# Optimization experiments

Measured on AMD Instinct MI355X. Metric: run time of the kernel, lower is better.

The kernel has to match this reference:

```python
import jax, jax.numpy as jnp
import numpy as np

N_NODES = 100000
N_EDGES = 1600000
NEG_SLOPE = 0.2
EPS = 1e-16


def gat_conv(x, edge_index, W, att_src, att_dst, bias, heads, out_ch, concat):
    # x: [N, F_in]; edge_index: [2, E] with edge (src j -> dst i)
    N = x.shape[0]
    src, dst = edge_index[0], edge_index[1]
    h = (x @ W).reshape(N, heads, out_ch)              # [N, H, C]
    a_src = (h * att_src[None]).sum(-1)                # [N, H]
    a_dst = (h * att_dst[None]).sum(-1)                # [N, H]
    e = a_src[src] + a_dst[dst]                        # [E, H]
    e = jnp.where(e > 0, e, NEG_SLOPE * e)             # LeakyReLU(0.2)
    # segment softmax over destination node
    m = jax.ops.segment_max(e, dst, num_segments=N)    # [N, H]
    m = jnp.where(jnp.isfinite(m), m, 0.0)
    ex = jnp.exp(e - m[dst])                           # [E, H]
    s = jax.ops.segment_sum(ex, dst, num_segments=N)   # [N, H]
    alpha = ex / (s[dst] + EPS)                        # [E, H]
    msg = h[src] * alpha[..., None]                    # [E, H, C]
    out = jax.ops.segment_sum(msg, dst, num_segments=N)  # [N, H, C]
    if concat:
        out = out.reshape(N, heads * out_ch)
    else:
        out = out.mean(axis=1)
    return out + bias


def setup_inputs() -> dict:
    key = jax.random.key(0)
    ks = jax.random.split(key, 8)
    x = jax.random.normal(ks[0], (N_NODES, 2), dtype=jnp.float32)
    edge_index = jax.random.randint(ks[1], (2, N_EDGES), 0, N_NODES, dtype=jnp.int64)
    glorot = lambda k, shape, fan: jax.random.normal(k, shape, jnp.float32) * (1.0 / np.sqrt(fan))
    W1 = glorot(ks[2], (2, 128), 2)
    att_src1 = glorot(ks[3], (8, 16), 16)
    att_dst1 = glorot(ks[4], (8, 16), 16)
    b1 = jnp.zeros((128,), jnp.float32)
    W2 = glorot(ks[5], (128, 4), 128)
    att_src2 = glorot(ks[6], (1, 4), 4)
    att_dst2 = glorot(ks[7], (1, 4), 4)
    b2 = jnp.zeros((4,), jnp.float32)
    return {"x": x, "edge_index": edge_index, "W1": W1, "att_src1": att_src1,
            "att_dst1": att_dst1, "b1": b1, "W2": W2, "att_src2": att_src2,
            "att_dst2": att_dst2, "b2": b2}


def reference(x, edge_index, W1, att_src1, att_dst1, b1, W2, att_src2, att_dst2, b2):
    h = gat_conv(x, edge_index, W1, att_src1, att_dst1, b1, heads=8, out_ch=16, concat=True)
    h = jax.nn.relu(h)
    # dropout p=0.6 is identity in eval mode
    h = gat_conv(h, edge_index, W2, att_src2, att_dst2, b2, heads=1, out_ch=4, concat=True)
    return jax.nn.log_softmax(h, axis=1)
```

## Files before the change

kernel.cpp:

```cpp
#include <hip/hip_runtime.h>
#include <math.h>

static constexpr float kNegSlope = 0.2f;
static constexpr float kEps = 1e-16f;
static constexpr int SLICES = 256;
static constexpr int BSHIFT = 7;
static constexpr int BMASK = 127;
static constexpr unsigned SRCMASK = 0x1FFFFu;
static constexpr int CAP = 2816;

__device__ __forceinline__ float leaky(float v) {
    return v > 0.0f ? v : kNegSlope * v;
}


__global__ __launch_bounds__(512) void k_hist1(const int* __restrict__ ei,
                                               int* __restrict__ table,
                                               int* __restrict__ rowptr,
                                               int E, int N, int NBUCK) {
    __shared__ int hist[832];
    int b = blockIdx.x, t = threadIdx.x;
    if (b == 0 && t == 0) rowptr[N] = E;
    for (int i = t; i < NBUCK; i += 512) hist[i] = 0;
    __syncthreads();
    int S = (((E + SLICES - 1) / SLICES) + 3) & ~3;
    int lo = b * S, hi = min(lo + S, E);
    for (int i = lo + t * 4; i < hi; i += 512 * 4) {
        int4 dv = *(const int4*)(ei + E + i);
        atomicAdd(&hist[dv.x >> BSHIFT], 1);
        atomicAdd(&hist[dv.y >> BSHIFT], 1);
        atomicAdd(&hist[dv.z >> BSHIFT], 1);
        atomicAdd(&hist[dv.w >> BSHIFT], 1);
    }
    __syncthreads();
    for (int i = t; i < NBUCK; i += 512) table[i * SLICES + b] = hist[i];
}

__global__ __launch_bounds__(256) void k_scan_reduce(const int* __restrict__ src,
                                                     int* __restrict__ partial, int n) {
    __shared__ int wsum[4];
    int b = blockIdx.x, t = threadIdx.x;
    int base = b * 1024 + t * 4;
    int s = 0;
#pragma unroll
    for (int k = 0; k < 4; ++k) {
        int idx = base + k;
        s += (idx < n) ? src[idx] : 0;
    }
#pragma unroll
    for (int off = 1; off < 64; off <<= 1) s += __shfl_xor(s, off);
    if ((t & 63) == 0) wsum[t >> 6] = s;
    __syncthreads();
    if (t == 0) partial[b] = wsum[0] + wsum[1] + wsum[2] + wsum[3];
}

__global__ __launch_bounds__(256) void k_scan_apply(int* __restrict__ data,
                                                    const int* __restrict__ partial,
                                                    int n, int nsb) {
    __shared__ int sm[8];
    __shared__ int baseSh;
    int b = blockIdx.x, t = threadIdx.x;
    int acc = 0;
    for (int i = t; i < b; i += 256) acc += partial[i];
#pragma unroll
    for (int off = 1; off < 64; off <<= 1) acc += __shfl_xor(acc, off);
    if ((t & 63) == 0) sm[t >> 6] = acc;
    __syncthreads();
    if (t == 0) baseSh = sm[0] + sm[1] + sm[2] + sm[3];
    __syncthreads();
    int chunkBase = baseSh;
    __syncthreads();
    int base = b * 1024 + t * 4;
    int v[4];
#pragma unroll
    for (int k = 0; k < 4; ++k) {
        int idx = base + k;
        v[k] = (idx < n) ? data[idx] : 0;
    }
    int sum4 = v[0] + v[1] + v[2] + v[3];
    int s = sum4;
#pragma unroll
    for (int off = 1; off < 64; off <<= 1) {
        int u = __shfl_up(s, off);
        if ((t & 63) >= off) s += u;
    }
    if ((t & 63) == 63) sm[t >> 6] = s;
    __syncthreads();
    int woff = 0;
    int w = t >> 6;
    for (int ww = 0; ww < w; ++ww) woff += sm[ww];
    int ex = chunkBase + woff + (s - sum4);
#pragma unroll
    for (int k = 0; k < 4; ++k) {
        int idx = base + k;
        if (idx < n) data[idx] = ex;
        ex += v[k];
    }
}

__global__ __launch_bounds__(512) void k_bin2(const int* __restrict__ ei,
                                              const int* __restrict__ table,
                                              unsigned* __restrict__ sbuf, int E, int NBUCK) {
    __shared__ int cur[832];
    int b = blockIdx.x, t = threadIdx.x;
    for (int i = t; i < NBUCK; i += 512) cur[i] = table[i * SLICES + b];
    __syncthreads();
    int S = (((E + SLICES - 1) / SLICES) + 3) & ~3;
    int lo = b * S, hi = min(lo + S, E);
    for (int i = lo + t * 4; i < hi; i += 512 * 4) {
        int4 sv = *(const int4*)(ei + i);
        int4 dv = *(const int4*)(ei + E + i);
        int pos;
        pos = atomicAdd(&cur[dv.x >> BSHIFT], 1);
        sbuf[pos] = (unsigned)sv.x | ((unsigned)(dv.x & BMASK) << 17);
        pos = atomicAdd(&cur[dv.y >> BSHIFT], 1);
        sbuf[pos] = (unsigned)sv.y | ((unsigned)(dv.y & BMASK) << 17);
        pos = atomicAdd(&cur[dv.z >> BSHIFT], 1);
        sbuf[pos] = (unsigned)sv.z | ((unsigned)(dv.z & BMASK) << 17);
        pos = atomicAdd(&cur[dv.w >> BSHIFT], 1);
        sbuf[pos] = (unsigned)sv.w | ((unsigned)(dv.w & BMASK) << 17);
    }
}

__global__ __launch_bounds__(512) void k_sort(
        const unsigned* __restrict__ sbuf, const int* __restrict__ table,
        int* __restrict__ rowptr, int* __restrict__ ssrc,
        int N, int E, int NBUCK) {
    __shared__ int hist[128];
    __shared__ int sc[128];
    __shared__ int cur[128];
    __shared__ unsigned raws[CAP];
    __shared__ int sls[CAP];
    int b = blockIdx.x;
    int t = threadIdx.x;
    int lo = table[b * SLICES];
    int hi = (b + 1 < NBUCK) ? table[(b + 1) * SLICES] : E;
    int cnt = hi - lo;
    bool inLds = (cnt <= CAP);

    if (t < 128) hist[t] = 0;
    __syncthreads();

    if (inLds) {
        for (int i = t; i < cnt; i += 512) {
            unsigned v = sbuf[lo + i];
            raws[i] = v;
            atomicAdd(&hist[v >> 17], 1);
        }
    } else {
        for (int i = lo + t; i < hi; i += 512) atomicAdd(&hist[sbuf[i] >> 17], 1);
    }
    __syncthreads();

    if (t < 128) {
        int lane = t & 63;
        int own = hist[t];
        int v = own;
#pragma unroll
        for (int off = 1; off < 64; off <<= 1) {
            int u = __shfl_up(v, off);
            if (lane >= off) v += u;
        }
        sc[t] = v;
    }
    __syncthreads();
    if (t < 128) {
        int ex = sc[t] - hist[t] + (t >= 64 ? sc[63] : 0);
        cur[t] = ex;
        int node = (b << BSHIFT) + t;
        if (node < N) rowptr[node] = lo + ex;
    }
    __syncthreads();

    if (inLds) {
        for (int i = t; i < cnt; i += 512) {
            unsigned v = raws[i];
            int pos = atomicAdd(&cur[v >> 17], 1);
            sls[pos] = (int)(v & SRCMASK);
        }
        __syncthreads();
        for (int i = t; i < cnt; i += 512) ssrc[lo + i] = sls[i];
    } else {
        for (int i = lo + t; i < hi; i += 512) {
            unsigned v = sbuf[i];
            int pos = atomicAdd(&cur[v >> 17], 1);
            ssrc[lo + pos] = (int)(v & SRCMASK);
        }
    }
}

__global__ __launch_bounds__(256) void k_gather1(
        const int* __restrict__ rowptr, const int* __restrict__ ssrc,
        const float* __restrict__ x,
        const float* __restrict__ W1, const float* __restrict__ att_src1,
        const float* __restrict__ att_dst1,
        float* __restrict__ attA, float* __restrict__ attB, int N) {
    __shared__ float pbuf[32];
    int t = threadIdx.x;
    if (t < 32) {
        int which = t >> 4;
        int hd = t & 15;
        int h = hd >> 1, d = hd & 1;
        const float* att = which ? att_dst1 : att_src1;
        float s = 0.0f;
#pragma unroll
        for (int c = 0; c < 16; ++c) s += W1[d * 128 + h * 16 + c] * att[h * 16 + c];
        pbuf[which * 16 + d * 8 + h] = s;
    }
    __syncthreads();

    int idx = blockIdx.x * blockDim.x + t;
    int n = idx >> 4;
    int sub = idx & 15;
    int h = sub & 7;
    int p = sub >> 3;
    if (n >= N) return;
    const float2* x2 = (const float2*)x;
    int start = rowptr[n], end = rowptr[n + 1];
    float2 xn = x2[n];
    float Ps0 = pbuf[h];
    float Ps1 = pbuf[8 + h];
    float adv = xn.x * pbuf[16 + h] + xn.y * pbuf[24 + h];
    float l = 0.f, s0 = 0.f, s1 = 0.f;
    int j = start + p;
    for (; j + 2 < end; j += 4) {
        int sa = ssrc[j];
        int sb = ssrc[j + 2];
        float2 xa = x2[sa];
        float2 xb = x2[sb];
        float pa = __expf(leaky(fmaf(xa.x, Ps0, fmaf(xa.y, Ps1, adv))));
        float pb = __expf(leaky(fmaf(xb.x, Ps0, fmaf(xb.y, Ps1, adv))));
        l += pa + pb;
        s0 = fmaf(pa, xa.x, fmaf(pb, xb.x, s0));
        s1 = fmaf(pa, xa.y, fmaf(pb, xb.y, s1));
    }
    if (j < end) {
        int sa = ssrc[j];
        float2 xa = x2[sa];
        float pa = __expf(leaky(fmaf(xa.x, Ps0, fmaf(xa.y, Ps1, adv))));
        l += pa;
        s0 = fmaf(pa, xa.x, s0);
        s1 = fmaf(pa, xa.y, s1);
    }
    l += __shfl_xor(l, 8);
    s0 += __shfl_xor(s0, 8);
    s1 += __shfl_xor(s1, 8);
    if (p == 0) {
        float inv = 1.0f / (l + kEps);
        attA[n * 8 + h] = s0 * inv;
        attB[n * 8 + h] = s1 * inv;
    }
}

__global__ __launch_bounds__(256) void k_fold(
        const float* __restrict__ attA, const float* __restrict__ attB,
        const float* __restrict__ W1, const float* __restrict__ b1,
        const float* __restrict__ W2, float* __restrict__ h2, int N) {
    __shared__ float4 pk1[128];
    __shared__ float4 pk2[128];
    int t = threadIdx.x;
    if (t < 128) {
        pk1[t] = make_float4(W1[t], W1[128 + t], b1[t], 0.f);
        pk2[t] = ((const float4*)W2)[t];
    }
    __syncthreads();
    int n = blockIdx.x * 256 + t;
    if (n >= N) return;
    const float4* A = (const float4*)(attA + n * 8);
    const float4* B = (const float4*)(attB + n * 8);
    float4 a01 = A[0], a23 = A[1];
    float4 b01 = B[0], b23 = B[1];
    float4 acc = make_float4(0.f, 0.f, 0.f, 0.f);
#pragma unroll
    for (int h = 0; h < 8; ++h) {
        float sx0 = (h == 0) ? a01.x : (h == 1) ? a01.y : (h == 2) ? a01.z :
                    (h == 3) ? a01.w : (h == 4) ? a23.x : (h == 5) ? a23.y :
                    (h == 6) ? a23.z : a23.w;
        float sx1 = (h == 0) ? b01.x : (h == 1) ? b01.y : (h == 2) ? b01.z :
                    (h == 3) ? b01.w : (h == 4) ? b23.x : (h == 5) ? b23.y :
                    (h == 6) ? b23.z : b23.w;
#pragma unroll
        for (int c = 0; c < 16; ++c) {
            int col = h * 16 + c;
            float4 p = pk1[col];
            float o = fmaxf(p.x * sx0 + p.y * sx1 + p.z, 0.0f);
            float4 w = pk2[col];
            acc.x += o * w.x;
            acc.y += o * w.y;
            acc.z += o * w.z;
            acc.w += o * w.w;
        }
    }
    ((float4*)h2)[n] = acc;
}

__global__ __launch_bounds__(256) void k_gather2_out(
        const int* __restrict__ rowptr, const int* __restrict__ ssrc,
        const float* __restrict__ h2, const float* __restrict__ att_src2,
        const float* __restrict__ att_dst2, const float* __restrict__ b2,
        float* __restrict__ out, int N) {
    int idx = blockIdx.x * blockDim.x + threadIdx.x;
    int n = idx >> 3, q = idx & 7;
    if (n >= N) return;
    int start = rowptr[n], end = rowptr[n + 1];
    float4 as2 = *(const float4*)att_src2;
    float4 ad2v = *(const float4*)att_dst2;
    const float4* h4 = (const float4*)h2;
    float4 hn = h4[n];
    float ad = hn.x * ad2v.x + hn.y * ad2v.y + hn.z * ad2v.z + hn.w * ad2v.w;
    float l = 0.0f;
    float4 acc = make_float4(0.f, 0.f, 0.f, 0.f);
    int j = start + q;
    for (; j + 8 < end; j += 16) {
        int s0 = ssrc[j];
        int s1 = ssrc[j + 8];
        float4 ha = h4[s0];
        float4 hb = h4[s1];
        float e0 = ha.x * as2.x + ha.y * as2.y + ha.z * as2.z + ha.w * as2.w + ad;
        float e1 = hb.x * as2.x + hb.y * as2.y + hb.z * as2.z + hb.w * as2.w + ad;
        float p0 = __expf(leaky(e0));
        float p1 = __expf(leaky(e1));
        l += p0 + p1;
        acc.x += p0 * ha.x + p1 * hb.x;
        acc.y += p0 * ha.y + p1 * hb.y;
        acc.z += p0 * ha.z + p1 * hb.z;
        acc.w += p0 * ha.w + p1 * hb.w;
    }
    if (j < end) {
        int s0 = ssrc[j];
        float4 ha = h4[s0];
        float e0 = ha.x * as2.x + ha.y * as2.y + ha.z * as2.z + ha.w * as2.w + ad;
        float p0 = __expf(leaky(e0));
        l += p0;
        acc.x += p0 * ha.x;
        acc.y += p0 * ha.y;
        acc.z += p0 * ha.z;
        acc.w += p0 * ha.w;
    }
#pragma unroll
    for (int off = 1; off < 8; off <<= 1) {
        l += __shfl_xor(l, off);
        acc.x += __shfl_xor(acc.x, off);
        acc.y += __shfl_xor(acc.y, off);
        acc.z += __shfl_xor(acc.z, off);
        acc.w += __shfl_xor(acc.w, off);
    }
    if (q == 0) {
        float inv = 1.0f / (l + kEps);
        float4 v = make_float4(acc.x * inv + b2[0], acc.y * inv + b2[1],
                               acc.z * inv + b2[2], acc.w * inv + b2[3]);
        float mx = fmaxf(fmaxf(v.x, v.y), fmaxf(v.z, v.w));
        float sum = __expf(v.x - mx) + __expf(v.y - mx) + __expf(v.z - mx) + __expf(v.w - mx);
        float lse = mx + logf(sum);
        ((float4*)out)[n] = make_float4(v.x - lse, v.y - lse, v.z - lse, v.w - lse);
    }
}

extern "C" void kernel_launch(void* const* d_in, const int* in_sizes, int n_in,
                              void* d_out, int out_size, void* d_ws, size_t ws_size,
                              hipStream_t stream) {
    const float* x        = (const float*)d_in[0];
    const int*   ei       = (const int*)d_in[1];
    const float* W1       = (const float*)d_in[2];
    const float* att_src1 = (const float*)d_in[3];
    const float* att_dst1 = (const float*)d_in[4];
    const float* b1       = (const float*)d_in[5];
    const float* W2       = (const float*)d_in[6];
    const float* att_src2 = (const float*)d_in[7];
    const float* att_dst2 = (const float*)d_in[8];
    const float* b2       = (const float*)d_in[9];

    const int N = in_sizes[0] / 2;
    const int E = in_sizes[1] / 2;
    const int NBUCK = (N + BMASK) >> BSHIFT;
    const int ntable = NBUCK * SLICES;
    const int nsb = (ntable + 1023) / 1024;

    int* table     = (int*)d_ws;
    int* partial   = table + ntable + 64;
    int* rowptr    = partial + 1024;
    int* ssrc      = rowptr + ((N + 4) & ~3);
    unsigned* sbuf = (unsigned*)(ssrc + E);
    float* attA    = (float*)sbuf;
    float* attB    = attA + (size_t)N * 8;
    size_t post    = (size_t)E > (size_t)N * 16 ? (size_t)E : (size_t)N * 16;
    float* h2      = (float*)(sbuf + post);

    k_hist1<<<SLICES, 512, 0, stream>>>(ei, table, rowptr, E, N, NBUCK);
    k_scan_reduce<<<nsb, 256, 0, stream>>>(table, partial, ntable);
    k_scan_apply<<<nsb, 256, 0, stream>>>(table, partial, ntable, nsb);
    k_bin2<<<SLICES, 512, 0, stream>>>(ei, table, sbuf, E, NBUCK);

    k_sort<<<NBUCK, 512, 0, stream>>>(sbuf, table, rowptr, ssrc, N, E, NBUCK);

    k_gather1<<<(N * 16 + 255) / 256, 256, 0, stream>>>(rowptr, ssrc, x,
                                                        W1, att_src1, att_dst1,
                                                        attA, attB, N);
    k_fold<<<(N + 255) / 256, 256, 0, stream>>>(attA, attB, W1, b1, W2, h2, N);

    k_gather2_out<<<(N * 8 + 255) / 256, 256, 0, stream>>>(rowptr, ssrc, h2,
                                                           att_src2, att_dst2, b2,
                                                           (float*)d_out, N);
}
```

Before: 151.6 us.

## Replace bucketed LDS counting sort with global-atomic CSR build

Builds the dst-sorted CSR with per-node global atomic counts, a scan over N, and a global-atomic scatter of source ids. This replaces the two-level bucket histogram, binning pass and per-bucket LDS sort. It removes two kernels and the intermediate packed buffer. The cost is 1.6M contended global atomics issued twice. Edge order within each row also becomes nondeterministic, which can change floating-point summation order.

```diff
diff --git a/kernel.cpp b/kernel.cpp
--- a/kernel.cpp
+++ b/kernel.cpp
@@ -3,37 +3,26 @@
 
 static constexpr float kNegSlope = 0.2f;
 static constexpr float kEps = 1e-16f;
-static constexpr int SLICES = 256;
-static constexpr int BSHIFT = 7;
-static constexpr int BMASK = 127;
-static constexpr unsigned SRCMASK = 0x1FFFFu;
-static constexpr int CAP = 2816;
 
 __device__ __forceinline__ float leaky(float v) {
     return v > 0.0f ? v : kNegSlope * v;
 }
 
 
-__global__ __launch_bounds__(512) void k_hist1(const int* __restrict__ ei,
-                                               int* __restrict__ table,
+__global__ __launch_bounds__(256) void k_count(const int* __restrict__ ei,
                                                int* __restrict__ rowptr,
-                                               int E, int N, int NBUCK) {
-    __shared__ int hist[832];
-    int b = blockIdx.x, t = threadIdx.x;
-    if (b == 0 && t == 0) rowptr[N] = E;
-    for (int i = t; i < NBUCK; i += 512) hist[i] = 0;
-    __syncthreads();
-    int S = (((E + SLICES - 1) / SLICES) + 3) & ~3;
-    int lo = b * S, hi = min(lo + S, E);
-    for (int i = lo + t * 4; i < hi; i += 512 * 4) {
-        int4 dv = *(const int4*)(ei + E + i);
-        atomicAdd(&hist[dv.x >> BSHIFT], 1);
-        atomicAdd(&hist[dv.y >> BSHIFT], 1);
-        atomicAdd(&hist[dv.z >> BSHIFT], 1);
-        atomicAdd(&hist[dv.w >> BSHIFT], 1);
-    }
-    __syncthreads();
-    for (int i = t; i < NBUCK; i += 512) table[i * SLICES + b] = hist[i];
+                                               int E, int N) {
+    if (blockIdx.x == 0 && threadIdx.x == 0) rowptr[N] = E;
+    int i4 = (blockIdx.x * 256 + threadIdx.x) * 4;
+    if (i4 + 3 < E) {
+        int4 dv = *(const int4*)(ei + E + i4);
+        atomicAdd(&rowptr[dv.x], 1);
+        atomicAdd(&rowptr[dv.y], 1);
+        atomicAdd(&rowptr[dv.z], 1);
+        atomicAdd(&rowptr[dv.w], 1);
+    } else {
+        for (int i = i4; i < E; ++i) atomicAdd(&rowptr[ei[E + i]], 1);
+    }
 }
 
 __global__ __launch_bounds__(256) void k_scan_reduce(const int* __restrict__ src,
@@ -55,6 +44,7 @@
 }
 
 __global__ __launch_bounds__(256) void k_scan_apply(int* __restrict__ data,
+                                                    int* __restrict__ cur,
                                                     const int* __restrict__ partial,
                                                     int n, int nsb) {
     __shared__ int sm[8];
@@ -93,98 +83,33 @@
 #pragma unroll
     for (int k = 0; k < 4; ++k) {
         int idx = base + k;
-        if (idx < n) data[idx] = ex;
+        if (idx < n) {
+            data[idx] = ex;
+            cur[idx] = ex;
+        }
         ex += v[k];
     }
 }
 
-__global__ __launch_bounds__(512) void k_bin2(const int* __restrict__ ei,
-                                              const int* __restrict__ table,
-                                              unsigned* __restrict__ sbuf, int E, int NBUCK) {
-    __shared__ int cur[832];
-    int b = blockIdx.x, t = threadIdx.x;
-    for (int i = t; i < NBUCK; i += 512) cur[i] = table[i * SLICES + b];
-    __syncthreads();
-    int S = (((E + SLICES - 1) / SLICES) + 3) & ~3;
-    int lo = b * S, hi = min(lo + S, E);
-    for (int i = lo + t * 4; i < hi; i += 512 * 4) {
-        int4 sv = *(const int4*)(ei + i);
-        int4 dv = *(const int4*)(ei + E + i);
-        int pos;
-        pos = atomicAdd(&cur[dv.x >> BSHIFT], 1);
-        sbuf[pos] = (unsigned)sv.x | ((unsigned)(dv.x & BMASK) << 17);
-        pos = atomicAdd(&cur[dv.y >> BSHIFT], 1);
-        sbuf[pos] = (unsigned)sv.y | ((unsigned)(dv.y & BMASK) << 17);
-        pos = atomicAdd(&cur[dv.z >> BSHIFT], 1);
-        sbuf[pos] = (unsigned)sv.z | ((unsigned)(dv.z & BMASK) << 17);
-        pos = atomicAdd(&cur[dv.w >> BSHIFT], 1);
-        sbuf[pos] = (unsigned)sv.w | ((unsigned)(dv.w & BMASK) << 17);
-    }
-}
-
-__global__ __launch_bounds__(512) void k_sort(
-        const unsigned* __restrict__ sbuf, const int* __restrict__ table,
-        int* __restrict__ rowptr, int* __restrict__ ssrc,
-        int N, int E, int NBUCK) {
-    __shared__ int hist[128];
-    __shared__ int sc[128];
-    __shared__ int cur[128];
-    __shared__ unsigned raws[CAP];
-    __shared__ int sls[CAP];
-    int b = blockIdx.x;
-    int t = threadIdx.x;
-    int lo = table[b * SLICES];
-    int hi = (b + 1 < NBUCK) ? table[(b + 1) * SLICES] : E;
-    int cnt = hi - lo;
-    bool inLds = (cnt <= CAP);
-
-    if (t < 128) hist[t] = 0;
-    __syncthreads();
-
-    if (inLds) {
-        for (int i = t; i < cnt; i += 512) {
-            unsigned v = sbuf[lo + i];
-            raws[i] = v;
-            atomicAdd(&hist[v >> 17], 1);
-        }
+__global__ __launch_bounds__(256) void k_scatter(const int* __restrict__ ei,
+                                                 int* __restrict__ cur,
+                                                 int* __restrict__ ssrc, int E) {
+    int i4 = (blockIdx.x * 256 + threadIdx.x) * 4;
+    if (i4 + 3 < E) {
+        int4 sv = *(const int4*)(ei + i4);
+        int4 dv = *(const int4*)(ei + E + i4);
+        int p0 = atomicAdd(&cur[dv.x], 1);
+        int p1 = atomicAdd(&cur[dv.y], 1);
+        int p2 = atomicAdd(&cur[dv.z], 1);
+        int p3 = atomicAdd(&cur[dv.w], 1);
+        ssrc[p0] = sv.x;
+        ssrc[p1] = sv.y;
+        ssrc[p2] = sv.z;
+        ssrc[p3] = sv.w;
     } else {
-        for (int i = lo + t; i < hi; i += 512) atomicAdd(&hist[sbuf[i] >> 17], 1);
-    }
-    __syncthreads();
-
-    if (t < 128) {
-        int lane = t & 63;
-        int own = hist[t];
-        int v = own;
-#pragma unroll
-        for (int off = 1; off < 64; off <<= 1) {
-            int u = __shfl_up(v, off);
-            if (lane >= off) v += u;
-        }
-        sc[t] = v;
-    }
-    __syncthreads();
-    if (t < 128) {
-        int ex = sc[t] - hist[t] + (t >= 64 ? sc[63] : 0);
-        cur[t] = ex;
-        int node = (b << BSHIFT) + t;
-        if (node < N) rowptr[node] = lo + ex;
-    }
-    __syncthreads();
-
-    if (inLds) {
-        for (int i = t; i < cnt; i += 512) {
-            unsigned v = raws[i];
-            int pos = atomicAdd(&cur[v >> 17], 1);
-            sls[pos] = (int)(v & SRCMASK);
-        }
-        __syncthreads();
-        for (int i = t; i < cnt; i += 512) ssrc[lo + i] = sls[i];
-    } else {
-        for (int i = lo + t; i < hi; i += 512) {
-            unsigned v = sbuf[i];
-            int pos = atomicAdd(&cur[v >> 17], 1);
-            ssrc[lo + pos] = (int)(v & SRCMASK);
+        for (int i = i4; i < E; ++i) {
+            int p = atomicAdd(&cur[ei[E + i]], 1);
+            ssrc[p] = ei[i];
         }
     }
 }
@@ -372,26 +297,22 @@
 
     const int N = in_sizes[0] / 2;
     const int E = in_sizes[1] / 2;
-    const int NBUCK = (N + BMASK) >> BSHIFT;
-    const int ntable = NBUCK * SLICES;
-    const int nsb = (ntable + 1023) / 1024;
-
-    int* table     = (int*)d_ws;
-    int* partial   = table + ntable + 64;
-    int* rowptr    = partial + 1024;
-    int* ssrc      = rowptr + ((N + 4) & ~3);
-    unsigned* sbuf = (unsigned*)(ssrc + E);
-    float* attA    = (float*)sbuf;
-    float* attB    = attA + (size_t)N * 8;
-    size_t post    = (size_t)E > (size_t)N * 16 ? (size_t)E : (size_t)N * 16;
-    float* h2      = (float*)(sbuf + post);
-
-    k_hist1<<<SLICES, 512, 0, stream>>>(ei, table, rowptr, E, N, NBUCK);
-    k_scan_reduce<<<nsb, 256, 0, stream>>>(table, partial, ntable);
-    k_scan_apply<<<nsb, 256, 0, stream>>>(table, partial, ntable, nsb);
-    k_bin2<<<SLICES, 512, 0, stream>>>(ei, table, sbuf, E, NBUCK);
-
-    k_sort<<<NBUCK, 512, 0, stream>>>(sbuf, table, rowptr, ssrc, N, E, NBUCK);
+    const int nsb = (N + 1023) / 1024;
+    const int eblocks = ((E + 3) / 4 + 255) / 256;
+
+    int* rowptr  = (int*)d_ws;
+    int* cur     = rowptr + ((N + 8) & ~3);
+    int* partial = cur + ((N + 4) & ~3);
+    int* ssrc    = partial + 1024;
+    float* attA  = (float*)(ssrc + E);
+    float* attB  = attA + (size_t)N * 8;
+    float* h2    = attB + (size_t)N * 8;
+
+    hipMemsetAsync(rowptr, 0, (size_t)N * sizeof(int), stream);
+    k_count<<<eblocks, 256, 0, stream>>>(ei, rowptr, E, N);
+    k_scan_reduce<<<nsb, 256, 0, stream>>>(rowptr, partial, N);
+    k_scan_apply<<<nsb, 256, 0, stream>>>(rowptr, cur, partial, N, nsb);
+    k_scatter<<<eblocks, 256, 0, stream>>>(ei, cur, ssrc, E);
 
     k_gather1<<<(N * 16 + 255) / 256, 256, 0, stream>>>(rowptr, ssrc, x,
                                                         W1, att_src1, att_dst1,
```

Measured after the change: 314.0 us. +107.1%, slower.

## Drop per-node sort; accumulate attention per bucket with LDS atomics

Applied to the files above, without the earlier changes.

Removes the per-bucket counting sort that built a CSR rowptr/ssrc. Both attention passes now run one block per 128-node bucket, scanning the unsorted bucket entries directly and accumulating softmax numerators and denominators into shared-memory arrays with float atomics. This eliminates a kernel launch and the ssrc/rowptr global writes and reads, but adds LDS atomic contention. Because float atomics run in no fixed order, summation order is no longer deterministic. Max-subtraction was already omitted before, so numerics are otherwise unchanged.

```diff
diff --git a/kernel.cpp b/kernel.cpp
--- a/kernel.cpp
+++ b/kernel.cpp
@@ -7,7 +7,6 @@
 static constexpr int BSHIFT = 7;
 static constexpr int BMASK = 127;
 static constexpr unsigned SRCMASK = 0x1FFFFu;
-static constexpr int CAP = 2816;
 
 __device__ __forceinline__ float leaky(float v) {
     return v > 0.0f ? v : kNegSlope * v;
@@ -16,11 +15,9 @@
 
 __global__ __launch_bounds__(512) void k_hist1(const int* __restrict__ ei,
                                                int* __restrict__ table,
-                                               int* __restrict__ rowptr,
-                                               int E, int N, int NBUCK) {
+                                               int E, int NBUCK) {
     __shared__ int hist[832];
     int b = blockIdx.x, t = threadIdx.x;
-    if (b == 0 && t == 0) rowptr[N] = E;
     for (int i = t; i < NBUCK; i += 512) hist[i] = 0;
     __syncthreads();
     int S = (((E + SLICES - 1) / SLICES) + 3) & ~3;
@@ -122,81 +119,20 @@
     }
 }
 
-__global__ __launch_bounds__(512) void k_sort(
+__global__ __launch_bounds__(512) void k_att1(
         const unsigned* __restrict__ sbuf, const int* __restrict__ table,
-        int* __restrict__ rowptr, int* __restrict__ ssrc,
-        int N, int E, int NBUCK) {
-    __shared__ int hist[128];
-    __shared__ int sc[128];
-    __shared__ int cur[128];
-    __shared__ unsigned raws[CAP];
-    __shared__ int sls[CAP];
-    int b = blockIdx.x;
-    int t = threadIdx.x;
-    int lo = table[b * SLICES];
-    int hi = (b + 1 < NBUCK) ? table[(b + 1) * SLICES] : E;
-    int cnt = hi - lo;
-    bool inLds = (cnt <= CAP);
-
-    if (t < 128) hist[t] = 0;
-    __syncthreads();
-
-    if (inLds) {
-        for (int i = t; i < cnt; i += 512) {
-            unsigned v = sbuf[lo + i];
-            raws[i] = v;
-            atomicAdd(&hist[v >> 17], 1);
-        }
-    } else {
-        for (int i = lo + t; i < hi; i += 512) atomicAdd(&hist[sbuf[i] >> 17], 1);
-    }
-    __syncthreads();
-
-    if (t < 128) {
-        int lane = t & 63;
-        int own = hist[t];
-        int v = own;
-#pragma unroll
-        for (int off = 1; off < 64; off <<= 1) {
-            int u = __shfl_up(v, off);
-            if (lane >= off) v += u;
-        }
-        sc[t] = v;
-    }
-    __syncthreads();
-    if (t < 128) {
-        int ex = sc[t] - hist[t] + (t >= 64 ? sc[63] : 0);
-        cur[t] = ex;
-        int node = (b << BSHIFT) + t;
-        if (node < N) rowptr[node] = lo + ex;
-    }
-    __syncthreads();
-
-    if (inLds) {
-        for (int i = t; i < cnt; i += 512) {
-            unsigned v = raws[i];
-            int pos = atomicAdd(&cur[v >> 17], 1);
-            sls[pos] = (int)(v & SRCMASK);
-        }
-        __syncthreads();
-        for (int i = t; i < cnt; i += 512) ssrc[lo + i] = sls[i];
-    } else {
-        for (int i = lo + t; i < hi; i += 512) {
-            unsigned v = sbuf[i];
-            int pos = atomicAdd(&cur[v >> 17], 1);
-            ssrc[lo + pos] = (int)(v & SRCMASK);
-        }
-    }
-}
-
-__global__ __launch_bounds__(256) void k_gather1(
-        const int* __restrict__ rowptr, const int* __restrict__ ssrc,
         const float* __restrict__ x,
         const float* __restrict__ W1, const float* __restrict__ att_src1,
         const float* __restrict__ att_dst1,
-        float* __restrict__ attA, float* __restrict__ attB, int N) {
+        float* __restrict__ attA, float* __restrict__ attB,
+        int N, int E, int NBUCK) {
     __shared__ float pbuf[32];
-    int t = threadIdx.x;
+    __shared__ float adv[1056];
+    __shared__ float accL[1056];
+    __shared__ float accS0[1056];
+    __shared__ float accS1[1056];
+    int b = blockIdx.x, t = threadIdx.x;
+    int base = b << BSHIFT;
     if (t < 32) {
         int which = t >> 4;
         int hd = t & 15;
@@ -207,48 +143,43 @@
         for (int c = 0; c < 16; ++c) s += W1[d * 128 + h * 16 + c] * att[h * 16 + c];
         pbuf[which * 16 + d * 8 + h] = s;
     }
-    __syncthreads();
-
-    int idx = blockIdx.x * blockDim.x + t;
-    int n = idx >> 4;
-    int sub = idx & 15;
-    int h = sub & 7;
-    int p = sub >> 3;
-    if (n >= N) return;
+    for (int i = t; i < 1056; i += 512) {
+        accL[i] = 0.f; accS0[i] = 0.f; accS1[i] = 0.f;
+    }
+    __syncthreads();
     const float2* x2 = (const float2*)x;
-    int start = rowptr[n], end = rowptr[n + 1];
-    float2 xn = x2[n];
-    float Ps0 = pbuf[h];
-    float Ps1 = pbuf[8 + h];
-    float adv = xn.x * pbuf[16 + h] + xn.y * pbuf[24 + h];
-    float l = 0.f, s0 = 0.f, s1 = 0.f;
-    int j = start + p;
-    for (; j + 2 < end; j += 4) {
-        int sa = ssrc[j];
-        int sb = ssrc[j + 2];
-        float2 xa = x2[sa];
-        float2 xb = x2[sb];
-        float pa = __expf(leaky(fmaf(xa.x, Ps0, fmaf(xa.y, Ps1, adv))));
-        float pb = __expf(leaky(fmaf(xb.x, Ps0, fmaf(xb.y, Ps1, adv))));
-        l += pa + pb;
-        s0 = fmaf(pa, xa.x, fmaf(pb, xb.x, s0));
-        s1 = fmaf(pa, xa.y, fmaf(pb, xb.y, s1));
-    }
-    if (j < end) {
-        int sa = ssrc[j];
-        float2 xa = x2[sa];
-        float pa = __expf(leaky(fmaf(xa.x, Ps0, fmaf(xa.y, Ps1, adv))));
-        l += pa;
-        s0 = fmaf(pa, xa.x, s0);
-        s1 = fmaf(pa, xa.y, s1);
-    }
-    l += __shfl_xor(l, 8);
-    s0 += __shfl_xor(s0, 8);
-    s1 += __shfl_xor(s1, 8);
-    if (p == 0) {
-        float inv = 1.0f / (l + kEps);
-        attA[n * 8 + h] = s0 * inv;
-        attB[n * 8 + h] = s1 * inv;
+    for (int e = t; e < 1024; e += 512) {
+        int h = e >> 7, d = e & 127;
+        int n = base + d;
+        float2 xn = (n < N) ? x2[n] : make_float2(0.f, 0.f);
+        adv[h * 132 + d] = xn.x * pbuf[16 + h] + xn.y * pbuf[24 + h];
+    }
+    __syncthreads();
+    int lo = table[b * SLICES];
+    int hi = (b + 1 < NBUCK) ? table[(b + 1) * SLICES] : E;
+    int h = t & 7;
+    float Ps0 = pbuf[h], Ps1 = pbuf[8 + h];
+    for (int j = lo + (t >> 3); j < hi; j += 64) {
+        unsigned v = sbuf[j];
+        int src = (int)(v & SRCMASK);
+        int d = (int)(v >> 17);
+        float2 xs = x2[src];
+        float p = __expf(leaky(fmaf(xs.x, Ps0, fmaf(xs.y, Ps1, adv[h * 132 + d]))));
+        int o = h * 132 + d;
+        atomicAdd(&accL[o], p);
+        atomicAdd(&accS0[o], p * xs.x);
+        atomicAdd(&accS1[o], p * xs.y);
+    }
+    __syncthreads();
+    for (int e = t; e < 1024; e += 512) {
+        int d = e >> 3, hh = e & 7;
+        int n = base + d;
+        if (n < N) {
+            int o = hh * 132 + d;
+            float inv = 1.0f / (accL[o] + kEps);
+            attA[n * 8 + hh] = accS0[o] * inv;
+            attB[n * 8 + hh] = accS1[o] * inv;
+        }
     }
 }
 
@@ -294,65 +225,61 @@
     ((float4*)h2)[n] = acc;
 }
 
-__global__ __launch_bounds__(256) void k_gather2_out(
-        const int* __restrict__ rowptr, const int* __restrict__ ssrc,
-        const float* __restrict__ h2, const float* __restrict__ att_src2,
+__global__ __launch_bounds__(512) void k_att2(
+        const unsigned* __restrict__ sbuf, const int* __restrict__ table,
+        const float* __restrict__ h2v, const float* __restrict__ att_src2,
         const float* __restrict__ att_dst2, const float* __restrict__ b2,
-        float* __restrict__ out, int N) {
-    int idx = blockIdx.x * blockDim.x + threadIdx.x;
-    int n = idx >> 3, q = idx & 7;
-    if (n >= N) return;
-    int start = rowptr[n], end = rowptr[n + 1];
+        float* __restrict__ out, int N, int E, int NBUCK) {
+    __shared__ float ad2[128];
+    __shared__ float acc[660];
+    int b = blockIdx.x, t = threadIdx.x;
+    int base = b << BSHIFT;
+    const float4* h4 = (const float4*)h2v;
     float4 as2 = *(const float4*)att_src2;
-    float4 ad2v = *(const float4*)att_dst2;
-    const float4* h4 = (const float4*)h2;
-    float4 hn = h4[n];
-    float ad = hn.x * ad2v.x + hn.y * ad2v.y + hn.z * ad2v.z + hn.w * ad2v.w;
-    float l = 0.0f;
-    float4 acc = make_float4(0.f, 0.f, 0.f, 0.f);
-    int j = start + q;
-    for (; j + 8 < end; j += 16) {
-        int s0 = ssrc[j];
-        int s1 = ssrc[j + 8];
-        float4 ha = h4[s0];
-        float4 hb = h4[s1];
-        float e0 = ha.x * as2.x + ha.y * as2.y + ha.z * as2.z + ha.w * as2.w + ad;
-        float e1 = hb.x * as2.x + hb.y * as2.y + hb.z * as2.z + hb.w * as2.w + ad;
-        float p0 = __expf(leaky(e0));
-        float p1 = __expf(leaky(e1));
-        l += p0 + p1;
-        acc.x += p0 * ha.x + p1 * hb.x;
-        acc.y += p0 * ha.y + p1 * hb.y;
-        acc.z += p0 * ha.z + p1 * hb.z;
-        acc.w += p0 * ha.w + p1 * hb.w;
-    }
-    if (j < end) {
-        int s0 = ssrc[j];
-        float4 ha = h4[s0];
-        float e0 = ha.x * as2.x + ha.y * as2.y + ha.z * as2.z + ha.w * as2.w + ad;
-        float p0 = __expf(leaky(e0));
-        l += p0;
-        acc.x += p0 * ha.x;
-        acc.y += p0 * ha.y;
-        acc.z += p0 * ha.z;
-        acc.w += p0 * ha.w;
-    }
-#pragma unroll
-    for (int off = 1; off < 8; off <<= 1) {
-        l += __shfl_xor(l, off);
-        acc.x += __shfl_xor(acc.x, off);
-        acc.y += __shfl_xor(acc.y, off);
-        acc.z += __shfl_xor(acc.z, off);
-        acc.w += __shfl_xor(acc.w, off);
-    }
-    if (q == 0) {
-        float inv = 1.0f / (l + kEps);
-        float4 v = make_float4(acc.x * inv + b2[0], acc.y * inv + b2[1],
-                               acc.z * inv + b2[2], acc.w * inv + b2[3]);
-        float mx = fmaxf(fmaxf(v.x, v.y), fmaxf(v.z, v.w));
-        float sum = __expf(v.x - mx) + __expf(v.y - mx) + __expf(v.z - mx) + __expf(v.w - mx);
-        float lse = mx + logf(sum);
-        ((float4*)out)[n] = make_float4(v.x - lse, v.y - lse, v.z - lse, v.w - lse);
+    for (int i = t; i < 660; i += 512) acc[i] = 0.f;
+    if (t < 128) {
+        int n = base + t;
+        if (n < N) {
+            float4 ad2v = *(const float4*)att_dst2;
+            float4 hn = h4[n];
+            ad2[t] = hn.x * ad2v.x + hn.y * ad2v.y + hn.z * ad2v.z + hn.w * ad2v.w;
+        } else {
+            ad2[t] = 0.f;
+        }
+    }
+    __syncthreads();
+    int lo = table[b * SLICES];
+    int hi = (b + 1 < NBUCK) ? table[(b + 1) * SLICES] : E;
+    for (int j = lo + t; j < hi; j += 512) {
+        unsigned v = sbuf[j];
+        int src = (int)(v & SRCMASK);
+        int d = (int)(v >> 17);
+        float4 hv = h4[src];
+        float e = fmaf(hv.x, as2.x, fmaf(hv.y, as2.y,
+                  fmaf(hv.z, as2.z, fmaf(hv.w, as2.w, ad2[d]))));
+        float p = __expf(leaky(e));
+        atomicAdd(&acc[d], p);
+        atomicAdd(&acc[132 + d], p * hv.x);
+        atomicAdd(&acc[264 + d], p * hv.y);
+        atomicAdd(&acc[396 + d], p * hv.z);
+        atomicAdd(&acc[528 + d], p * hv.w);
+    }
+    __syncthreads();
+    if (t < 128) {
+        int n = base + t;
+        if (n < N) {
+            float inv = 1.0f / (acc[t] + kEps);
+            float4 v4 = make_float4(acc[132 + t] * inv + b2[0],
+                                    acc[264 + t] * inv + b2[1],
+                                    acc[396 + t] * inv + b2[2],
+                                    acc[528 + t] * inv + b2[3]);
+            float mx = fmaxf(fmaxf(v4.x, v4.y), fmaxf(v4.z, v4.w));
+            float sum = __expf(v4.x - mx) + __expf(v4.y - mx) +
+                        __expf(v4.z - mx) + __expf(v4.w - mx);
+            float lse = mx + logf(sum);
+            ((float4*)out)[n] = make_float4(v4.x - lse, v4.y - lse,
+                                            v4.z - lse, v4.w - lse);
+        }
     }
 }
 
@@ -378,27 +305,20 @@
 
     int* table     = (int*)d_ws;
     int* partial   = table + ntable + 64;
-    int* rowptr    = partial + 1024;
-    int* ssrc      = rowptr + ((N + 4) & ~3);
-    unsigned* sbuf = (unsigned*)(ssrc + E);
-    float* attA    = (float*)sbuf;
+    unsigned* sbuf = (unsigned*)(partial + 1024);
+    float* attA    = (float*)(sbuf + E);
     float* attB    = attA + (size_t)N * 8;
-    size_t post    = (size_t)E > (size_t)N * 16 ? (size_t)E : (size_t)N * 16;
-    float* h2      = (float*)(sbuf + post);
-
-    k_hist1<<<SLICES, 512, 0, stream>>>(ei, table, rowptr, E, N, NBUCK);
+    float* h2      = attB + (size_t)N * 8;
+
+    k_hist1<<<SLICES, 512, 0, stream>>>(ei, table, E, NBUCK);
     k_scan_reduce<<<nsb, 256, 0, stream>>>(table, partial, ntable);
     k_scan_apply<<<nsb, 256, 0, stream>>>(table, partial, ntable, nsb);
     k_bin2<<<SLICES, 512, 0, stream>>>(ei, table, sbuf, E, NBUCK);
 
-    k_sort<<<NBUCK, 512, 0, stream>>>(sbuf, table, rowptr, ssrc, N, E, NBUCK);
-
-    k_gather1<<<(N * 16 + 255) / 256, 256, 0, stream>>>(rowptr, ssrc, x,
-                                                        W1, att_src1, att_dst1,
-                                                        attA, attB, N);
+    k_att1<<<NBUCK, 512, 0, stream>>>(sbuf, table, x, W1, att_src1, att_dst1,
+                                      attA, attB, N, E, NBUCK);
     k_fold<<<(N + 255) / 256, 256, 0, stream>>>(attA, attB, W1, b1, W2, h2, N);
 
-    k_gather2_out<<<(N * 8 + 255) / 256, 256, 0, stream>>>(rowptr, ssrc, h2,
-                                                           att_src2, att_dst2, b2,
-                                                           (float*)d_out, N);
-}
+    k_att2<<<NBUCK, 512, 0, stream>>>(sbuf, table, h2, att_src2, att_dst2, b2,
+                                      (float*)d_out, N, E, NBUCK);
+}
```

Result: slower. 421.9 us (+178.3%).
